# Kernel optimization log

Measured on AMD Instinct MI355X. Metric: run time of the kernel, lower is better.

Reference implementation:

```python
import jax, jax.numpy as jnp
import numpy as np

B, S, D = 8, 2048, 2048  # seq_len must equal dim for this module's math to type-check


def setup_inputs() -> dict:
    key = jax.random.key(0)
    ks = jax.random.split(key, 9)
    sc = 1.0 / np.sqrt(D)
    return {
        "query": jax.random.normal(ks[0], (B, S, D), jnp.float32),
        "key_": jax.random.normal(ks[1], (B, S, D), jnp.float32),
        "value": jax.random.normal(ks[2], (B, S, D), jnp.float32),
        "Wq": jax.random.normal(ks[3], (D, D), jnp.float32) * sc,
        "bq": jax.random.normal(ks[4], (D,), jnp.float32) * 0.01,
        "Wk": jax.random.normal(ks[5], (D, D), jnp.float32) * sc,
        "bk": jax.random.normal(ks[6], (D,), jnp.float32) * 0.01,
        "Wv": jax.random.normal(ks[7], (D, D), jnp.float32) * sc,
        "bv": jax.random.normal(ks[8], (D,), jnp.float32) * 0.01,
    }


def reference(query, key_, value, Wq, bq, Wk, bk, Wv, bv):
    scale_factor = 1.0  # forward default
    # Linear projections (torch Linear: x @ W^T + b)
    q = jnp.einsum('bsd,ed->bse', query, Wq) + bq   # [B,S,D]
    k = jnp.einsum('bsd,ed->bse', key_, Wk) + bk    # [B,S,D]
    v = jnp.einsum('bsd,ed->bse', value, Wv) + bv   # [B,S,D]
    # Transpose last two dims, then matmul: [B,D,S] @ [B,D,S] (valid since S == D)
    qT = jnp.swapaxes(q, -2, -1)
    kT = jnp.swapaxes(k, -2, -1)
    qk = jnp.matmul(qT, kT) * scale_factor          # [B,D,S]
    attn = jax.nn.softmax(qk, axis=-1)
    # dropout_p = 0 -> identity
    out = jnp.matmul(attn, v)                       # [B,D,D]
    return jnp.swapaxes(out, -2, -1)
```

## Files before the change

kernel.cpp:

```cpp
#include <hip/hip_runtime.h>
#include <hip/hip_fp16.h>


using half8_t = __attribute__((ext_vector_type(8))) _Float16;
using f32x4   = __attribute__((ext_vector_type(4))) float;

static constexpr int NB = 8;
static constexpr int Sd = 2048;
static constexpr long MAT = (long)Sd * Sd;

__device__ __forceinline__ void gload16(const _Float16* g, _Float16* l) {
  __builtin_amdgcn_global_load_lds(
      (const __attribute__((address_space(1))) void*)g,
      (__attribute__((address_space(3))) void*)l, 16, 0, 0);
}
__device__ __forceinline__ void barrier_() { asm volatile("s_barrier" ::: "memory"); }
__device__ __forceinline__ void lgkm0_()   { asm volatile("s_waitcnt lgkmcnt(0)" ::: "memory"); }
#define VMCNT(n) asm volatile("s_waitcnt vmcnt(" #n ")" ::: "memory")
#define SCHEDB() __builtin_amdgcn_sched_barrier(0)

template<bool SPLIT>
__global__ __launch_bounds__(256) void presplit(const float* __restrict__ in,
    _Float16* __restrict__ h, _Float16* __restrict__ l, long n8, float scl)
{
  long i = (long)blockIdx.x * 256 + threadIdx.x;
  const long stride = (long)gridDim.x * 256;
  for (; i < n8; i += stride) {
    const f32x4* p = (const f32x4*)(in + i * 8);
    f32x4 a = p[0], b = p[1];
    half8_t hh, ll;
#pragma unroll
    for (int j = 0; j < 4; j++) {
      float x = a[j] * scl; _Float16 hv = (_Float16)x;
      hh[j] = hv; if constexpr (SPLIT) ll[j] = (_Float16)(x - (float)hv);
      float y = b[j] * scl; _Float16 hw = (_Float16)y;
      hh[4 + j] = hw; if constexpr (SPLIT) ll[4 + j] = (_Float16)(y - (float)hw);
    }
    *(half8_t*)(h + i * 8) = hh;
    if constexpr (SPLIT) *(half8_t*)(l + i * 8) = ll;
  }
}

__device__ __forceinline__ void lda4(const _Float16* unit, int off, int fmhOff,
                                     half8_t (&a)[4]) {
#pragma unroll
  for (int f = 0; f < 4; f++)
    a[f] = *(const half8_t*)((const char*)unit + off + fmhOff + f * 1024);
}

template<int FMH>
__device__ __forceinline__ void mm16(f32x4 (&acc)[8][4], const half8_t (&a)[4],
                                     const half8_t (&b)[4]) {
  __builtin_amdgcn_s_setprio(1);
#pragma unroll
  for (int f = 0; f < 4; f++)
#pragma unroll
    for (int n = 0; n < 4; n++)
      acc[FMH * 4 + f][n] =
          __builtin_amdgcn_mfma_f32_16x16x32_f16(a[f], b[n], acc[FMH * 4 + f][n], 0, 0, 0);
  __builtin_amdgcn_s_setprio(0);
}

template<int NSEG, int BIAS, int OUT>
__global__ __launch_bounds__(512, 2) void gemm7(
    const _Float16* __restrict__ Ah, const _Float16* __restrict__ Al, long sA,
    const _Float16* __restrict__ Bh, long sB,
    const float* __restrict__ bias, float cscale,
    void* __restrict__ Cp, void* __restrict__ Clp, long sC)
{
  constexpr int H = NSEG * 64;
  __shared__ __align__(16) _Float16 LA[4][8192];
  __shared__ __align__(16) _Float16 LB[4][8192];

  const int t = threadIdx.x, w = t >> 6, l = t & 63;

  const int wg = blockIdx.x;
  const int swz = (wg & 7) * 64 + (wg >> 3);
  const int bz = swz >> 6, rem = swz & 63;
  const int by = rem >> 3, bx = rem & 7;

  const _Float16* PAh = Ah + (size_t)bz * sA + (size_t)(by * 256) * Sd;
  const _Float16* PBh = Bh + (size_t)bz * sB + (size_t)(bx * 256) * Sd;
  const _Float16* PAl = (NSEG == 2)
      ? Al + (size_t)bz * sA + (size_t)(by * 256) * Sd : PAh;

  const int s7 = t & 7;
  const int lkS = (s7 >> 1) ^ ((t >> 3) & 3);
  const size_t srcoff = (size_t)(2 * (t >> 3) + (s7 & 1)) * Sd + lkS * 8;
  const int du0 = w * 512;

  const int wm = (w >> 2) * 128, wn = (w & 3) * 64;
  const int lm = l & 15, lkr = l >> 4;
  const int sprime = ((lkr ^ ((lm >> 1) & 3)) << 1) | (lm & 1);
  const int aoff = (wm >> 1) * 128 + (lm >> 1) * 128 + sprime * 16;
  const int boff = (wn >> 1) * 128 + (lm >> 1) * 128 + sprime * 16;

  auto srcA = [&](int hp) -> const _Float16* {
    if constexpr (NSEG == 2) return (hp >> 6) ? PAl : PAh;
    return PAh;
  };
  auto koOf = [&](int hp) -> int {
    if constexpr (NSEG == 2) return (hp & 63) * 32;
    return hp * 32;
  };
  auto stageA2 = [&](int hp) {
    const int uu = hp & 3;
    const _Float16* a = srcA(hp) + koOf(hp);
    gload16(a + srcoff, LA[uu] + du0);
    gload16(a + srcoff + (size_t)128 * Sd, LA[uu] + du0 + 4096);
  };
  auto stageB2 = [&](int hp) {
    const int uu = hp & 3;
    const _Float16* b = PBh + koOf(hp);
    gload16(b + srcoff, LB[uu] + du0);
    gload16(b + srcoff + (size_t)128 * Sd, LB[uu] + du0 + 4096);
  };

  f32x4 acc[8][4] = {};
  half8_t fa[4], fb[4];

  stageA2(0); stageB2(0); stageA2(1); stageB2(1); stageA2(2); stageB2(2);
  VMCNT(8);
  barrier_();

  for (int u = 0; u < H; ++u) {
    const int slot = u & 3;
    const bool st = (u + 3 < H);
    lda4(LA[slot], aoff, 0, fa);
    lda4(LB[slot], boff, 0, fb);
    if (st) stageA2(u + 3);
    barrier_();
    lgkm0_(); SCHEDB();
    mm16<0>(acc, fa, fb);
    barrier_();
    lda4(LA[slot], aoff, 4096, fa);
    if (st) stageB2(u + 3);
    if (u + 3 < H)      { VMCNT(8); }
    else if (u + 2 < H) { VMCNT(4); }
    else if (u + 1 < H) { VMCNT(0); }
    barrier_();
    lgkm0_(); SCHEDB();
    mm16<1>(acc, fa, fb);
    barrier_();
  }

  const int row_base = by * 256 + wm + (lkr << 2);
  const int col_base = bx * 256 + wn + lm;
#pragma unroll
  for (int fm = 0; fm < 8; fm++)
#pragma unroll
    for (int fn = 0; fn < 4; fn++) {
      const int n = col_base + fn * 16;
      float bcol = 0.f;
      if constexpr (BIAS == 1) bcol = bias[n];
#pragma unroll
      for (int r = 0; r < 4; r++) {
        const int m = row_base + fm * 16 + r;
        float v = acc[fm][fn][r] * cscale;
        if constexpr (BIAS == 1) v += bcol;
        if constexpr (BIAS == 2) v += bias[m];
        const size_t ci = (size_t)bz * sC + (size_t)m * Sd + n;
        if constexpr (OUT == 0) ((float*)Cp)[ci] = v;
        else if constexpr (OUT == 1) ((_Float16*)Cp)[ci] = (_Float16)v;
        else if constexpr (OUT == 3) ((_Float16*)Cp)[ci] = (_Float16)(v * 16.0f);
        else {
          float sv = v * 16.0f;
          _Float16 hv = (_Float16)sv;
          ((_Float16*)Cp)[ci]  = hv;
          ((_Float16*)Clp)[ci] = (_Float16)(sv - (float)hv);
        }
      }
    }
}

__global__ __launch_bounds__(256) void softmax_rows(const float* __restrict__ X,
                                                    _Float16* __restrict__ P)
{
  __shared__ float red[4];
  const size_t row = blockIdx.x;
  const float* x = X + row * Sd;
  _Float16* p = P + row * Sd;
  const int t = threadIdx.x;
  float v[8];
  float mx = -1e30f;
#pragma unroll
  for (int i = 0; i < 8; i++) { v[i] = x[t + 256 * i]; mx = fmaxf(mx, v[i]); }
#pragma unroll
  for (int o = 32; o > 0; o >>= 1) mx = fmaxf(mx, __shfl_xor(mx, o, 64));
  if ((t & 63) == 0) red[t >> 6] = mx;
  __syncthreads();
  mx = fmaxf(fmaxf(red[0], red[1]), fmaxf(red[2], red[3]));
  __syncthreads();
  float s = 0.f;
#pragma unroll
  for (int i = 0; i < 8; i++) { v[i] = __expf(v[i] - mx); s += v[i]; }
#pragma unroll
  for (int o = 32; o > 0; o >>= 1) s += __shfl_xor(s, o, 64);
  if ((t & 63) == 0) red[t >> 6] = s;
  __syncthreads();
  s = red[0] + red[1] + red[2] + red[3];
  float inv = 1.f / s;
#pragma unroll
  for (int i = 0; i < 8; i++) p[t + 256 * i] = (_Float16)(v[i] * inv);
}

extern "C" void kernel_launch(void* const* d_in, const int* in_sizes, int n_in,
                              void* d_out, int out_size, void* d_ws, size_t ws_size,
                              hipStream_t stream)
{
  const float* query = (const float*)d_in[0];
  const float* key_  = (const float*)d_in[1];
  const float* value = (const float*)d_in[2];
  const float* Wq = (const float*)d_in[3];
  const float* bq = (const float*)d_in[4];
  const float* Wk = (const float*)d_in[5];
  const float* bk = (const float*)d_in[6];
  const float* Wv = (const float*)d_in[7];
  const float* bv = (const float*)d_in[8];

  char* ws = (char*)d_ws;
  char* ob = (char*)d_out;
  const size_t M64 = (size_t)NB * MAT * 2;

  _Float16* q_h  = (_Float16*)(ws);
  _Float16* k_h  = (_Float16*)(ws);
  _Float16* k_l  = (_Float16*)(ws + M64);
  float*    qk   = (float*)(ws);
  _Float16* qT_h = (_Float16*)(ws + 2 * M64);
  _Float16* qT_l = (_Float16*)(ws + 3 * M64);
  _Float16* P    = qT_h;
  _Float16* vT   = qT_l;
  _Float16* kk_h = (_Float16*)(ws + 4 * M64);
  _Float16* val_h = (_Float16*)(ws + 5 * M64);

  _Float16* wq_h = (_Float16*)(ob);
  _Float16* wq_l = (_Float16*)(ob + (MAT * 2));
  _Float16* wk_h = (_Float16*)(ob + 2 * (MAT * 2));
  _Float16* wv_h = (_Float16*)(ob + 3 * (MAT * 2));
  float* out = (float*)d_out;

  dim3 blk256(256), blk512(512);
  dim3 gg(512);
  const long NQ8 = (long)NB * MAT / 8;
  const long NW8 = MAT / 8;

  presplit<false><<<dim3(2048), blk256, 0, stream>>>(query, q_h, nullptr, NQ8, 16.f);
  presplit<true><<<dim3(2048), blk256, 0, stream>>>(Wq, wq_h, wq_l, NW8, 16.f);
  gemm7<2, 2, 2><<<gg, blk512, 0, stream>>>(wq_h, wq_l, 0, q_h, MAT,
                                            bq, 1.f / 256.f, qT_h, qT_l, MAT);
  presplit<true><<<dim3(2048), blk256, 0, stream>>>(key_, k_h, k_l, NQ8, 16.f);
  presplit<false><<<dim3(2048), blk256, 0, stream>>>(Wk, wk_h, nullptr, NW8, 16.f);
  gemm7<2, 1, 3><<<gg, blk512, 0, stream>>>(k_h, k_l, MAT, wk_h, 0,
                                            bk, 1.f / 256.f, kk_h, nullptr, MAT);
  gemm7<2, 0, 0><<<gg, blk512, 0, stream>>>(qT_h, qT_l, MAT, kk_h, MAT,
                                            nullptr, 1.f / 256.f, qk, nullptr, MAT);
  softmax_rows<<<dim3(NB * Sd), blk256, 0, stream>>>(qk, P);
  presplit<false><<<dim3(2048), blk256, 0, stream>>>(value, val_h, nullptr, NQ8, 1.f);
  presplit<false><<<dim3(2048), blk256, 0, stream>>>(Wv, wv_h, nullptr, NW8, 1.f);
  gemm7<1, 2, 1><<<gg, blk512, 0, stream>>>(wv_h, nullptr, 0, val_h, MAT,
                                            bv, 1.f, vT, nullptr, MAT);
  gemm7<1, 0, 0><<<gg, blk512, 0, stream>>>(vT, nullptr, MAT, P, MAT,
                                            nullptr, 1.f, out, nullptr, MAT);
}
```

Measured before the change: 1.293 ms.

## Double-buffer register fragments and halve barriers per k-step in GEMM main loop

Rewrites the GEMM main loop so LDS fragments for the next k-step are read into a second register set while the current step's 32 MFMAs run, unrolled by two. It merges the A and B staging into one call and cuts the barriers per k-step from four to one, using compiler builtins in place of inline-asm barriers and waits. The aim is to hide LDS read latency and remove synchronisation stalls. The cost is higher register pressure from two full fragment sets, which could threaten the 2-blocks-per-CU launch bound, and the more subtle slot reuse ordering carries some risk.

```diff
diff --git a/kernel.cpp b/kernel.cpp
--- a/kernel.cpp
+++ b/kernel.cpp
@@ -14,9 +14,8 @@
       (const __attribute__((address_space(1))) void*)g,
       (__attribute__((address_space(3))) void*)l, 16, 0, 0);
 }
-__device__ __forceinline__ void barrier_() { asm volatile("s_barrier" ::: "memory"); }
-__device__ __forceinline__ void lgkm0_()   { asm volatile("s_waitcnt lgkmcnt(0)" ::: "memory"); }
-#define VMCNT(n) asm volatile("s_waitcnt vmcnt(" #n ")" ::: "memory")
+#define VMCNT(n) asm volatile("s_waitcnt vmcnt(" #n ")")
+#define BAR()    __builtin_amdgcn_s_barrier()
 #define SCHEDB() __builtin_amdgcn_sched_barrier(0)
 
 template<bool SPLIT>
@@ -41,28 +40,8 @@
   }
 }
 
-__device__ __forceinline__ void lda4(const _Float16* unit, int off, int fmhOff,
-                                     half8_t (&a)[4]) {
-#pragma unroll
-  for (int f = 0; f < 4; f++)
-    a[f] = *(const half8_t*)((const char*)unit + off + fmhOff + f * 1024);
-}
-
-template<int FMH>
-__device__ __forceinline__ void mm16(f32x4 (&acc)[8][4], const half8_t (&a)[4],
-                                     const half8_t (&b)[4]) {
-  __builtin_amdgcn_s_setprio(1);
-#pragma unroll
-  for (int f = 0; f < 4; f++)
-#pragma unroll
-    for (int n = 0; n < 4; n++)
-      acc[FMH * 4 + f][n] =
-          __builtin_amdgcn_mfma_f32_16x16x32_f16(a[f], b[n], acc[FMH * 4 + f][n], 0, 0, 0);
-  __builtin_amdgcn_s_setprio(0);
-}
-
 template<int NSEG, int BIAS, int OUT>
-__global__ __launch_bounds__(512, 2) void gemm7(
+__global__ __launch_bounds__(512, 2) void gemm8(
     const _Float16* __restrict__ Ah, const _Float16* __restrict__ Al, long sA,
     const _Float16* __restrict__ Bh, long sB,
     const float* __restrict__ bias, float cscale,
@@ -103,45 +82,62 @@
     if constexpr (NSEG == 2) return (hp & 63) * 32;
     return hp * 32;
   };
-  auto stageA2 = [&](int hp) {
+  auto stageU = [&](int hp) {
     const int uu = hp & 3;
     const _Float16* a = srcA(hp) + koOf(hp);
+    const _Float16* b = PBh + koOf(hp);
     gload16(a + srcoff, LA[uu] + du0);
     gload16(a + srcoff + (size_t)128 * Sd, LA[uu] + du0 + 4096);
-  };
-  auto stageB2 = [&](int hp) {
-    const int uu = hp & 3;
-    const _Float16* b = PBh + koOf(hp);
     gload16(b + srcoff, LB[uu] + du0);
     gload16(b + srcoff + (size_t)128 * Sd, LB[uu] + du0 + 4096);
   };
 
   f32x4 acc[8][4] = {};
-  half8_t fa[4], fb[4];
-
-  stageA2(0); stageB2(0); stageA2(1); stageB2(1); stageA2(2); stageB2(2);
-  VMCNT(8);
-  barrier_();
-
-  for (int u = 0; u < H; ++u) {
-    const int slot = u & 3;
-    const bool st = (u + 3 < H);
-    lda4(LA[slot], aoff, 0, fa);
-    lda4(LB[slot], boff, 0, fb);
-    if (st) stageA2(u + 3);
-    barrier_();
-    lgkm0_(); SCHEDB();
-    mm16<0>(acc, fa, fb);
-    barrier_();
-    lda4(LA[slot], aoff, 4096, fa);
-    if (st) stageB2(u + 3);
-    if (u + 3 < H)      { VMCNT(8); }
-    else if (u + 2 < H) { VMCNT(4); }
-    else if (u + 1 < H) { VMCNT(0); }
-    barrier_();
-    lgkm0_(); SCHEDB();
-    mm16<1>(acc, fa, fb);
-    barrier_();
+  half8_t a0[8], b0[4], a1[8], b1[4];
+
+  auto readF = [&](int slot, half8_t (&fa)[8], half8_t (&fb)[4]) {
+#pragma unroll
+    for (int f = 0; f < 8; f++)
+      fa[f] = *(const half8_t*)((const char*)LA[slot] + aoff + f * 1024);
+#pragma unroll
+    for (int n = 0; n < 4; n++)
+      fb[n] = *(const half8_t*)((const char*)LB[slot] + boff + n * 1024);
+  };
+  auto mfma32 = [&](const half8_t (&fa)[8], const half8_t (&fb)[4]) {
+    __builtin_amdgcn_s_setprio(1);
+#pragma unroll
+    for (int f = 0; f < 8; f++)
+#pragma unroll
+      for (int n = 0; n < 4; n++)
+        acc[f][n] = __builtin_amdgcn_mfma_f32_16x16x32_f16(fa[f], fb[n], acc[f][n], 0, 0, 0);
+    __builtin_amdgcn_s_setprio(0);
+  };
+
+  stageU(0); stageU(1); stageU(2);
+  VMCNT(4);
+  BAR();
+  readF(0, a0, b0);
+
+  for (int j = 0; j < H / 2; ++j) {
+    {
+      const int u = 2 * j;
+      readF((u + 1) & 3, a1, b1);
+      SCHEDB();
+      mfma32(a0, b0);
+      SCHEDB();
+      if (u + 3 < H) { stageU(u + 3); VMCNT(4); }
+      BAR();
+    }
+    {
+      const int u = 2 * j + 1;
+      if (u + 1 < H) readF((u + 1) & 3, a0, b0);
+      SCHEDB();
+      mfma32(a1, b1);
+      SCHEDB();
+      if (u + 3 < H)      { stageU(u + 3); VMCNT(4); }
+      else if (u == H - 3) { VMCNT(0); }
+      if (u + 1 < H) BAR();
+    }
   }
 
   const int row_base = by * 256 + wm + (lkr << 2);
@@ -246,19 +242,19 @@
 
   presplit<false><<<dim3(2048), blk256, 0, stream>>>(query, q_h, nullptr, NQ8, 16.f);
   presplit<true><<<dim3(2048), blk256, 0, stream>>>(Wq, wq_h, wq_l, NW8, 16.f);
-  gemm7<2, 2, 2><<<gg, blk512, 0, stream>>>(wq_h, wq_l, 0, q_h, MAT,
+  gemm8<2, 2, 2><<<gg, blk512, 0, stream>>>(wq_h, wq_l, 0, q_h, MAT,
                                             bq, 1.f / 256.f, qT_h, qT_l, MAT);
   presplit<true><<<dim3(2048), blk256, 0, stream>>>(key_, k_h, k_l, NQ8, 16.f);
   presplit<false><<<dim3(2048), blk256, 0, stream>>>(Wk, wk_h, nullptr, NW8, 16.f);
-  gemm7<2, 1, 3><<<gg, blk512, 0, stream>>>(k_h, k_l, MAT, wk_h, 0,
+  gemm8<2, 1, 3><<<gg, blk512, 0, stream>>>(k_h, k_l, MAT, wk_h, 0,
                                             bk, 1.f / 256.f, kk_h, nullptr, MAT);
-  gemm7<2, 0, 0><<<gg, blk512, 0, stream>>>(qT_h, qT_l, MAT, kk_h, MAT,
+  gemm8<2, 0, 0><<<gg, blk512, 0, stream>>>(qT_h, qT_l, MAT, kk_h, MAT,
                                             nullptr, 1.f / 256.f, qk, nullptr, MAT);
   softmax_rows<<<dim3(NB * Sd), blk256, 0, stream>>>(qk, P);
   presplit<false><<<dim3(2048), blk256, 0, stream>>>(value, val_h, nullptr, NQ8, 1.f);
   presplit<false><<<dim3(2048), blk256, 0, stream>>>(Wv, wv_h, nullptr, NW8, 1.f);
-  gemm7<1, 2, 1><<<gg, blk512, 0, stream>>>(wv_h, nullptr, 0, val_h, MAT,
+  gemm8<1, 2, 1><<<gg, blk512, 0, stream>>>(wv_h, nullptr, 0, val_h, MAT,
                                             bv, 1.f, vT, nullptr, MAT);
-  gemm7<1, 0, 0><<<gg, blk512, 0, stream>>>(vT, nullptr, MAT, P, MAT,
+  gemm8<1, 0, 0><<<gg, blk512, 0, stream>>>(vT, nullptr, MAT, P, MAT,
                                             nullptr, 1.f, out, nullptr, MAT);
 }
```

After: 1.265 ms. -2.1%, faster.

## Shrink GEMM tile to 128x256 with double-buffered single-barrier pipeline

Applied to the files above, without the earlier changes.

Replaces the 256x256 tile GEMM, which used a 4-stage LDS ring and two half-steps per k-iteration, with a 128x256 tile using 2-stage double buffering and one barrier per k-step. The grid doubles to 1024 workgroups and launch bounds allow 4 blocks per CU, trading per-block reuse and prefetch depth for more occupancy and less LDS per block. The A-operand staging layout and swizzle are reworked for the narrower tile. The risk is lower arithmetic intensity per block and a VMCNT(0) wait every iteration, which can expose memory latency.

```diff
diff --git a/kernel.cpp b/kernel.cpp
--- a/kernel.cpp
+++ b/kernel.cpp
@@ -41,61 +41,43 @@
   }
 }
 
-__device__ __forceinline__ void lda4(const _Float16* unit, int off, int fmhOff,
-                                     half8_t (&a)[4]) {
-#pragma unroll
-  for (int f = 0; f < 4; f++)
-    a[f] = *(const half8_t*)((const char*)unit + off + fmhOff + f * 1024);
-}
-
-template<int FMH>
-__device__ __forceinline__ void mm16(f32x4 (&acc)[8][4], const half8_t (&a)[4],
-                                     const half8_t (&b)[4]) {
-  __builtin_amdgcn_s_setprio(1);
-#pragma unroll
-  for (int f = 0; f < 4; f++)
-#pragma unroll
-    for (int n = 0; n < 4; n++)
-      acc[FMH * 4 + f][n] =
-          __builtin_amdgcn_mfma_f32_16x16x32_f16(a[f], b[n], acc[FMH * 4 + f][n], 0, 0, 0);
-  __builtin_amdgcn_s_setprio(0);
-}
-
 template<int NSEG, int BIAS, int OUT>
-__global__ __launch_bounds__(512, 2) void gemm7(
+__global__ __launch_bounds__(512, 4) void gemm11(
     const _Float16* __restrict__ Ah, const _Float16* __restrict__ Al, long sA,
     const _Float16* __restrict__ Bh, long sB,
     const float* __restrict__ bias, float cscale,
     void* __restrict__ Cp, void* __restrict__ Clp, long sC)
 {
   constexpr int H = NSEG * 64;
-  __shared__ __align__(16) _Float16 LA[4][8192];
-  __shared__ __align__(16) _Float16 LB[4][8192];
+  __shared__ __align__(16) _Float16 LA[2][4096];
+  __shared__ __align__(16) _Float16 LB[2][8192];
 
   const int t = threadIdx.x, w = t >> 6, l = t & 63;
 
   const int wg = blockIdx.x;
-  const int swz = (wg & 7) * 64 + (wg >> 3);
-  const int bz = swz >> 6, rem = swz & 63;
+  const int swz = (wg & 7) * 128 + (wg >> 3);
+  const int bz = swz >> 7, rem = swz & 127;
   const int by = rem >> 3, bx = rem & 7;
 
-  const _Float16* PAh = Ah + (size_t)bz * sA + (size_t)(by * 256) * Sd;
+  const _Float16* PAh = Ah + (size_t)bz * sA + (size_t)(by * 128) * Sd;
   const _Float16* PBh = Bh + (size_t)bz * sB + (size_t)(bx * 256) * Sd;
   const _Float16* PAl = (NSEG == 2)
-      ? Al + (size_t)bz * sA + (size_t)(by * 256) * Sd : PAh;
-
+      ? Al + (size_t)bz * sA + (size_t)(by * 128) * Sd : PAh;
+
+  const size_t srcA_off = (size_t)(t >> 2) * Sd
+                        + (size_t)(((t & 3) ^ ((t >> 3) & 3)) * 8);
   const int s7 = t & 7;
-  const int lkS = (s7 >> 1) ^ ((t >> 3) & 3);
-  const size_t srcoff = (size_t)(2 * (t >> 3) + (s7 & 1)) * Sd + lkS * 8;
+  const size_t srcB_off = (size_t)(2 * (t >> 3) + (s7 & 1)) * Sd
+                        + (size_t)(((s7 >> 1) ^ ((t >> 3) & 3)) * 8);
   const int du0 = w * 512;
 
-  const int wm = (w >> 2) * 128, wn = (w & 3) * 64;
+  const int wm = (w >> 2) * 64, wn = (w & 3) * 64;
   const int lm = l & 15, lkr = l >> 4;
+  const int aoff = wm * 64 + lm * 64 + ((lkr ^ ((lm >> 1) & 3)) * 16);
   const int sprime = ((lkr ^ ((lm >> 1) & 3)) << 1) | (lm & 1);
-  const int aoff = (wm >> 1) * 128 + (lm >> 1) * 128 + sprime * 16;
   const int boff = (wn >> 1) * 128 + (lm >> 1) * 128 + sprime * 16;
 
-  auto srcA = [&](int hp) -> const _Float16* {
+  auto srcAh = [&](int hp) -> const _Float16* {
     if constexpr (NSEG == 2) return (hp >> 6) ? PAl : PAh;
     return PAh;
   };
@@ -103,51 +85,47 @@
     if constexpr (NSEG == 2) return (hp & 63) * 32;
     return hp * 32;
   };
-  auto stageA2 = [&](int hp) {
-    const int uu = hp & 3;
-    const _Float16* a = srcA(hp) + koOf(hp);
-    gload16(a + srcoff, LA[uu] + du0);
-    gload16(a + srcoff + (size_t)128 * Sd, LA[uu] + du0 + 4096);
+  auto stageP = [&](int hp) {
+    const int u = hp & 1;
+    const _Float16* a = srcAh(hp) + koOf(hp);
+    const _Float16* b = PBh + koOf(hp);
+    gload16(a + srcA_off, LA[u] + du0);
+    gload16(b + srcB_off, LB[u] + du0);
+    gload16(b + srcB_off + (size_t)128 * Sd, LB[u] + du0 + 4096);
   };
-  auto stageB2 = [&](int hp) {
-    const int uu = hp & 3;
-    const _Float16* b = PBh + koOf(hp);
-    gload16(b + srcoff, LB[uu] + du0);
-    gload16(b + srcoff + (size_t)128 * Sd, LB[uu] + du0 + 4096);
-  };
-
-  f32x4 acc[8][4] = {};
+
+  f32x4 acc[4][4] = {};
   half8_t fa[4], fb[4];
 
-  stageA2(0); stageB2(0); stageA2(1); stageB2(1); stageA2(2); stageB2(2);
-  VMCNT(8);
+  stageP(0);
+  VMCNT(0);
   barrier_();
 
   for (int u = 0; u < H; ++u) {
-    const int slot = u & 3;
-    const bool st = (u + 3 < H);
-    lda4(LA[slot], aoff, 0, fa);
-    lda4(LB[slot], boff, 0, fb);
-    if (st) stageA2(u + 3);
-    barrier_();
+    if (u + 1 < H) stageP(u + 1);
+    const int s = u & 1;
+#pragma unroll
+    for (int f = 0; f < 4; f++)
+      fa[f] = *(const half8_t*)((const char*)LA[s] + aoff + f * 1024);
+#pragma unroll
+    for (int n = 0; n < 4; n++)
+      fb[n] = *(const half8_t*)((const char*)LB[s] + boff + n * 1024);
     lgkm0_(); SCHEDB();
-    mm16<0>(acc, fa, fb);
-    barrier_();
-    lda4(LA[slot], aoff, 4096, fa);
-    if (st) stageB2(u + 3);
-    if (u + 3 < H)      { VMCNT(8); }
-    else if (u + 2 < H) { VMCNT(4); }
-    else if (u + 1 < H) { VMCNT(0); }
-    barrier_();
-    lgkm0_(); SCHEDB();
-    mm16<1>(acc, fa, fb);
-    barrier_();
+    __builtin_amdgcn_s_setprio(1);
+#pragma unroll
+    for (int fm = 0; fm < 4; fm++)
+#pragma unroll
+      for (int fn = 0; fn < 4; fn++)
+        acc[fm][fn] = __builtin_amdgcn_mfma_f32_16x16x32_f16(
+            fa[fm], fb[fn], acc[fm][fn], 0, 0, 0);
+    __builtin_amdgcn_s_setprio(0);
+    if (u + 1 < H) { VMCNT(0); barrier_(); }
   }
 
-  const int row_base = by * 256 + wm + (lkr << 2);
+  const int row_base = by * 128 + wm + (lkr << 2);
   const int col_base = bx * 256 + wn + lm;
 #pragma unroll
-  for (int fm = 0; fm < 8; fm++)
+  for (int fm = 0; fm < 4; fm++)
 #pragma unroll
     for (int fn = 0; fn < 4; fn++) {
       const int n = col_base + fn * 16;
@@ -240,25 +218,25 @@
   float* out = (float*)d_out;
 
   dim3 blk256(256), blk512(512);
-  dim3 gg(512);
+  dim3 gg(1024);
   const long NQ8 = (long)NB * MAT / 8;
   const long NW8 = MAT / 8;
 
   presplit<false><<<dim3(2048), blk256, 0, stream>>>(query, q_h, nullptr, NQ8, 16.f);
   presplit<true><<<dim3(2048), blk256, 0, stream>>>(Wq, wq_h, wq_l, NW8, 16.f);
-  gemm7<2, 2, 2><<<gg, blk512, 0, stream>>>(wq_h, wq_l, 0, q_h, MAT,
-                                            bq, 1.f / 256.f, qT_h, qT_l, MAT);
+  gemm11<2, 2, 2><<<gg, blk512, 0, stream>>>(wq_h, wq_l, 0, q_h, MAT,
+                                             bq, 1.f / 256.f, qT_h, qT_l, MAT);
   presplit<true><<<dim3(2048), blk256, 0, stream>>>(key_, k_h, k_l, NQ8, 16.f);
   presplit<false><<<dim3(2048), blk256, 0, stream>>>(Wk, wk_h, nullptr, NW8, 16.f);
-  gemm7<2, 1, 3><<<gg, blk512, 0, stream>>>(k_h, k_l, MAT, wk_h, 0,
-                                            bk, 1.f / 256.f, kk_h, nullptr, MAT);
-  gemm7<2, 0, 0><<<gg, blk512, 0, stream>>>(qT_h, qT_l, MAT, kk_h, MAT,
-                                            nullptr, 1.f / 256.f, qk, nullptr, MAT);
+  gemm11<2, 1, 3><<<gg, blk512, 0, stream>>>(k_h, k_l, MAT, wk_h, 0,
+                                             bk, 1.f / 256.f, kk_h, nullptr, MAT);
+  gemm11<2, 0, 0><<<gg, blk512, 0, stream>>>(qT_h, qT_l, MAT, kk_h, MAT,
+                                             nullptr, 1.f / 256.f, qk, nullptr, MAT);
   softmax_rows<<<dim3(NB * Sd), blk256, 0, stream>>>(qk, P);
   presplit<false><<<dim3(2048), blk256, 0, stream>>>(value, val_h, nullptr, NQ8, 1.f);
   presplit<false><<<dim3(2048), blk256, 0, stream>>>(Wv, wv_h, nullptr, NW8, 1.f);
-  gemm7<1, 2, 1><<<gg, blk512, 0, stream>>>(wv_h, nullptr, 0, val_h, MAT,
-                                            bv, 1.f, vT, nullptr, MAT);
-  gemm7<1, 0, 0><<<gg, blk512, 0, stream>>>(vT, nullptr, MAT, P, MAT,
-                                            nullptr, 1.f, out, nullptr, MAT);
-}
+  gemm11<1, 2, 1><<<gg, blk512, 0, stream>>>(wv_h, nullptr, 0, val_h, MAT,
+                                             bv, 1.f, vT, nullptr, MAT);
+  gemm11<1, 0, 0><<<gg, blk512, 0, stream>>>(vT, nullptr, MAT, P, MAT,
+                                             nullptr, 1.f, out, nullptr, MAT);
+}
```

New measurement: 1.336 ms. 1.03x slower.
